# Performance work log

Hardware: AMD Instinct MI355X
Metric: run time of the kernel (lower is better)

The kernel has to match this reference:

```python
import jax, jax.numpy as jnp
import numpy as np

PRIME = 2147483647  # 2^31 - 1, MinHash modulus
GAMMA = 0.3
NUM_HEADS = 8


def minhash_sketch(ids, a, b):
    # ids: (B, L, S) int64 atom ids; a,b: (K,) hash coefficients
    # h[b,l,s,k] = (a[k]*id + b[k]) mod PRIME ; signature = min over the set axis S
    h = (ids[..., None] * a + b) % PRIME          # (B, L, S, K)
    return h.min(axis=2)                          # (B, L, K)


def jaccard_from_signatures(sig_q, sig_k):
    # sig_q: (B, Lq, K), sig_k: (B, Lk, K) -> (B, Lq, Lk) fraction of matching slots.
    # Scan over the K hash slots to avoid materializing a (B,Lq,Lk,K) tensor.
    B, Lq, K = sig_q.shape
    Lk = sig_k.shape[1]

    def step(acc, cols):
        qc, kc = cols                              # (B,Lq), (B,Lk)
        return acc + (qc[:, :, None] == kc[:, None, :]).astype(jnp.float32), None

    init = jnp.zeros((B, Lq, Lk), jnp.float32)
    xs = (jnp.moveaxis(sig_q, -1, 0), jnp.moveaxis(sig_k, -1, 0))
    acc, _ = jax.lax.scan(step, init, xs)
    return acc / K


def symdiff_from_jaccard(jacc, size_q, size_k):
    # |A ∩ B| = J/(1+J) * (|A|+|B|)  =>  |A Δ B| = (|A|+|B|) * (1-J)/(1+J)
    tot = size_q[:, :, None] + size_k[:, None, :]   # (B, Lq, Lk)
    return tot * (1.0 - jacc) / (1.0 + jacc)


def setup_inputs() -> dict:
    key = jax.random.key(0)
    ks = jax.random.split(key, 12)
    B, Lq, Lk, E, S, K, V = 4, 1024, 1024, 512, 8, 128, 32000
    w = lambda k: (jax.random.normal(k, (E, E), jnp.float32) * 0.02)
    return {
        "query": jax.random.normal(ks[0], (B, Lq, E), jnp.float32),
        "key": jax.random.normal(ks[1], (B, Lk, E), jnp.float32),
        "value": jax.random.normal(ks[2], (B, Lk, E), jnp.float32),
        "token_sets_q": jax.random.randint(ks[3], (B, Lq, S), 0, V).astype(jnp.int64),
        "token_sets_k": jax.random.randint(ks[4], (B, Lk, S), 0, V).astype(jnp.int64),
        "hash_a": jax.random.randint(ks[5], (K,), 1, PRIME - 1).astype(jnp.int64),
        "hash_b": jax.random.randint(ks[6], (K,), 0, PRIME - 1).astype(jnp.int64),
        "Wq": w(ks[7]), "bq": jnp.zeros((E,), jnp.float32),
        "Wk": w(ks[8]), "bk": jnp.zeros((E,), jnp.float32),
        "Wv": w(ks[9]), "bv": jnp.zeros((E,), jnp.float32),
        "Wo": w(ks[10]), "bo": jnp.zeros((E,), jnp.float32),
    }


def reference(query, key, value, token_sets_q, token_sets_k, hash_a, hash_b,
              Wq, bq, Wk, bk, Wv, bv, Wo, bo):
    B, Lq, E = query.shape
    Lk = key.shape[1]
    H = NUM_HEADS
    d = E // H

    # in-projections (torch Linear: x @ W^T + b); q,k are computed but the
    # attention scores come solely from the token-set kernel (gating disabled)
    q = query @ Wq.T + bq
    k = key @ Wk.T + bk
    v = (value @ Wv.T + bv).reshape(B, Lk, H, d).transpose(0, 2, 1, 3)  # (B,H,Lk,d)

    # MinHash sketches of per-token atom sets -> estimated Jaccard -> Δ-RBF score
    sig_q = minhash_sketch(token_sets_q, hash_a, hash_b)   # (B,Lq,K)
    sig_k = minhash_sketch(token_sets_k, hash_a, hash_b)   # (B,Lk,K)
    jacc = jaccard_from_signatures(sig_q, sig_k)           # (B,Lq,Lk)

    S = token_sets_q.shape[-1]
    size_q = jnp.full((B, Lq), S, jnp.float32)             # uniform CSR offsets -> |set| = S
    size_k = jnp.full((B, Lk), S, jnp.float32)
    delta = symdiff_from_jaccard(jacc, size_q, size_k)
    scores = jnp.exp(-GAMMA * delta)                       # (B,Lq,Lk), shared by all heads

    attn = jax.nn.softmax(scores, axis=-1)                 # no masks, no causal, dropout=0
    ctx = jnp.einsum('bqk,bhkd->bqhd', attn, v).reshape(B, Lq, E)
    return ctx @ Wo.T + bo
```

## Files before the change

### kernel.cpp

```cpp
#include <hip/hip_runtime.h>
#include <hip/hip_bf16.h>
#include <stdint.h>

#define PRIME 2147483647u
#define GAMMA 0.3f
#define K_HASH 128
#define S_SET 8
#define NB 4
#define LQ 1024
#define LK 1024
#define EDIM 512

typedef unsigned short ushort_t;
typedef __attribute__((ext_vector_type(8))) short short8;
typedef __attribute__((ext_vector_type(4))) float f32x4;

static __device__ __forceinline__ unsigned short f2bf(float f) {
    unsigned u = __builtin_bit_cast(unsigned, f);
    u += 0x7FFFu + ((u >> 16) & 1u);
    return (unsigned short)(u >> 16);
}

static __device__ __forceinline__ void glds16(const void* g, void* l) {
    __builtin_amdgcn_global_load_lds(
        (const __attribute__((address_space(1))) unsigned int*)g,
        (__attribute__((address_space(3))) unsigned int*)l, 16, 0, 0);
}

#define SWZ(r) ((((r) >> 2) & 3) ^ ((r) & 3))

static __device__ __forceinline__ unsigned nm2(unsigned acc, unsigned a,
                                               unsigned b, unsigned ones) {
    unsigned x = a ^ b, t;
    asm("v_pk_min_u16 %0, %1, %2" : "=v"(t) : "v"(x), "v"(ones));
    return acc + t;
}
static __device__ __forceinline__ unsigned nm8(unsigned acc, int4 q, int4 k,
                                               unsigned ones) {
    acc = nm2(acc, (unsigned)q.x, (unsigned)k.x, ones);
    acc = nm2(acc, (unsigned)q.y, (unsigned)k.y, ones);
    acc = nm2(acc, (unsigned)q.z, (unsigned)k.z, ones);
    acc = nm2(acc, (unsigned)q.w, (unsigned)k.w, ones);
    return acc;
}

#define EPI_ROWBIAS  0
#define EPI_ROWDIV   1
#define EPI_COLBIAS  2

template<int OUTF32, int MODE>
static __device__ void gemm64_dev(
        const ushort_t* __restrict__ A, const ushort_t* __restrict__ B,
        void* __restrict__ C,
        const float* __restrict__ bias, const float* __restrict__ scale,
        int lda, int ldb, int ldc, int Kd, int m0, int n0,
        ushort_t* AsBase, ushort_t* BsBase, int tid) {
    ushort_t (*As)[64 * 32] = (ushort_t (*)[64 * 32])AsBase;
    ushort_t (*Bs)[64 * 32] = (ushort_t (*)[64 * 32])BsBase;
    int w = tid >> 6, lane = tid & 63;
    int wm = (w & 1) * 32, wn = (w >> 1) * 32;
    int mrow = lane & 15, kg = lane >> 4;

    int r = tid >> 2, c = (tid & 3) ^ SWZ(r);
    const ushort_t* pa = A + (size_t)(m0 + r) * lda + c * 8;
    const ushort_t* pb = B + (size_t)(n0 + r) * ldb + c * 8;

    int aoff[2], boff[2];
    #pragma unroll
    for (int s = 0; s < 2; s++) {
        int Ra = wm + s * 16 + mrow;
        aoff[s] = Ra * 32 + (kg ^ SWZ(Ra)) * 8;
        int Rb = wn + s * 16 + mrow;
        boff[s] = Rb * 32 + (kg ^ SWZ(Rb)) * 8;
    }

    f32x4 acc[2][2] = {};
    int nK = Kd >> 5;
    glds16(pa, &As[0][tid * 8]);
    glds16(pb, &Bs[0][tid * 8]);
    for (int i = 0; i < nK; i++) {
        __syncthreads();
        int cur = i & 1, nxt = cur ^ 1;
        if (i + 1 < nK) {
            int k0 = (i + 1) << 5;
            glds16(pa + k0, &As[nxt][tid * 8]);
            glds16(pb + k0, &Bs[nxt][tid * 8]);
        }
        short8 af[2], bh[2];
        #pragma unroll
        for (int s = 0; s < 2; s++) {
            af[s] = *(const short8*)&As[cur][aoff[s]];
            bh[s] = *(const short8*)&Bs[cur][boff[s]];
        }
        #pragma unroll
        for (int ii = 0; ii < 2; ii++)
            #pragma unroll
            for (int jj = 0; jj < 2; jj++)
                acc[ii][jj] = __builtin_amdgcn_mfma_f32_16x16x32_bf16(
                                  af[ii], bh[jj], acc[ii][jj], 0, 0, 0);
    }

    int col = lane & 15, rbase = (lane >> 4) * 4;
    #pragma unroll
    for (int ii = 0; ii < 2; ii++) {
        #pragma unroll
        for (int jj = 0; jj < 2; jj++) {
            #pragma unroll
            for (int rr = 0; rr < 4; rr++) {
                int gm = m0 + wm + ii * 16 + rbase + rr;
                int gn = n0 + wn + jj * 16 + col;
                float v = acc[ii][jj][rr];
                if (MODE == EPI_ROWBIAS)     v += bias[gm];
                else if (MODE == EPI_ROWDIV) v /= scale[gm];
                else                         v += bias[gn];
                size_t cix = (size_t)gm * ldc + gn;
                if (OUTF32) ((float*)C)[cix] = v;
                else        ((ushort_t*)C)[cix] = f2bf(v);
            }
        }
    }
}

#define CVT_N0 (NB * LK * EDIM)
#define CVT_N1 (EDIM * EDIM)
#define CVT_N2 (EDIM * EDIM)
#define CVT_BLOCKS ((CVT_N0 + CVT_N1 + CVT_N2) / (256 * 8))
#define SIG_BLOCKS (NB * (LQ + LK) / 2)

__global__ __launch_bounds__(256) void prep_kernel(
        const float* __restrict__ v, const float* __restrict__ wv,
        const float* __restrict__ wo,
        ushort_t* __restrict__ vb, ushort_t* __restrict__ wvb,
        ushort_t* __restrict__ wob,
        const int* __restrict__ ts_q, const int* __restrict__ ts_k,
        const int* __restrict__ ha, const int* __restrict__ hb,
        ushort_t* __restrict__ sig_q, ushort_t* __restrict__ sig_k,
        float* __restrict__ rs) {
    int blk = blockIdx.x;
    if (blk < CVT_BLOCKS) {
        size_t i = ((size_t)blk * 256 + threadIdx.x) * 8;
        const float* src; ushort_t* dst; size_t off;
        if (i < CVT_N0)                { src = v;  dst = vb;  off = i; }
        else if (i < CVT_N0 + CVT_N1)  { src = wv; dst = wvb; off = i - CVT_N0; }
        else                           { src = wo; dst = wob; off = i - CVT_N0 - CVT_N1; }
        float4 a = *(const float4*)(src + off);
        float4 b = *(const float4*)(src + off + 4);
        ushort4 o0, o1;
        o0.x = f2bf(a.x); o0.y = f2bf(a.y); o0.z = f2bf(a.z); o0.w = f2bf(a.w);
        o1.x = f2bf(b.x); o1.y = f2bf(b.y); o1.z = f2bf(b.z); o1.w = f2bf(b.w);
        *(ushort4*)(dst + off)     = o0;
        *(ushort4*)(dst + off + 4) = o1;
        return;
    }
    int sb = blk - CVT_BLOCKS;
    if (sb < 16) rs[sb * 256 + threadIdx.x] = 0.f;
    int half = threadIdx.x >> 7, k = threadIdx.x & 127;
    int row = sb * 2 + half;
    const int* ts = (row < NB * LQ) ? ts_q : ts_k;
    ushort_t* sig = (row < NB * LQ) ? sig_q : sig_k;
    int idx = row & (NB * LQ - 1);
    unsigned long long a  = (unsigned)ha[k];
    unsigned long long bb = (unsigned)hb[k];
    __shared__ int ids[2][S_SET];
    if (k < S_SET) ids[half][k] = ts[idx * S_SET + k];
    __syncthreads();
    unsigned mn = 0xFFFFFFFFu;
    #pragma unroll
    for (int s = 0; s < S_SET; s++) {
        unsigned long long x = a * (unsigned long long)(unsigned)ids[half][s] + bb;
        x = (x & PRIME) + (x >> 31);
        x = (x & PRIME) + (x >> 31);
        unsigned r = (unsigned)x;
        if (r >= PRIME) r -= PRIME;
        mn = (r < mn) ? r : mn;
    }
    sig[idx * K_HASH + k] = (ushort_t)mn;
}

union JacSmem {
    struct {
        int Qs[128 * 36];
        int Ks[64 * 36];
        float lut[K_HASH + 1];
    } jac;
    struct {
        ushort_t As[2][64 * 32];
        ushort_t Bs[2][64 * 32];
    } g;
};

__global__ __launch_bounds__(256) void jacg1_kernel(
        const ushort_t* __restrict__ sig_q, const ushort_t* __restrict__ sig_k,
        ushort_t* __restrict__ P, float* __restrict__ rs,
        const ushort_t* __restrict__ Wvb, const ushort_t* __restrict__ Vb,
        ushort_t* __restrict__ Vt, const float* __restrict__ bv) {
    __shared__ JacSmem sm;
    int blk = blockIdx.x, tid = threadIdx.x;
    int grp = blk >> 8;
    int t = (grp >> 1) * 256 + (blk & 255);
    if (grp & 1) {
        gemm64_dev<0, EPI_ROWBIAS>(Wvb, Vb, Vt, bv, nullptr,
                                   EDIM, EDIM, NB * LK, EDIM,
                                   (t >> 6) * 64, (t & 63) * 64,
                                   sm.g.As[0], sm.g.Bs[0], tid);
        return;
    }
    if (tid <= K_HASH) {
        float r = (float)(K_HASH - tid) / (float)(K_HASH + tid);
        sm.jac.lut[tid] = expf(expf(-GAMMA * (2.0f * S_SET) * r));
    }
    int b = t >> 7;
    int q0 = ((t >> 4) & 7) * 128, j0 = (t & 15) * 64;
    const int4* gq = (const int4*)(sig_q + ((size_t)b * LQ + q0) * K_HASH);
    const int4* gk = (const int4*)(sig_k + ((size_t)b * LK + j0) * K_HASH);
    int tx = tid & 15, ty = tid >> 4;
    unsigned ones = 0x00010001u;
    unsigned acc[8][4] = {};
    int sra = tid >> 2, srb = 64 + sra, sg0 = (tid & 3) * 2;
    #pragma unroll 1
    for (int h = 0; h < 2; h++) {
        __syncthreads();
        #pragma unroll
        for (int u = 0; u < 2; u++) {
            int g = sg0 + u;
            *(int4*)&sm.jac.Qs[sra * 36 + ((g ^ (sra >> 2)) & 7) * 4]
                = gq[sra * 16 + h * 8 + g];
            *(int4*)&sm.jac.Qs[srb * 36 + ((g ^ (srb >> 2)) & 7) * 4]
                = gq[srb * 16 + h * 8 + g];
            *(int4*)&sm.jac.Ks[sra * 36 + ((g ^ (sra >> 2)) & 7) * 4]
                = gk[sra * 16 + h * 8 + g];
        }
        __syncthreads();
        #pragma unroll
        for (int g = 0; g < 8; g++) {
            int4 qv[8], kv[4];
            #pragma unroll
            for (int i = 0; i < 8; i++) {
                int r = ty * 8 + i;
                qv[i] = *(const int4*)&sm.jac.Qs[r * 36 + ((g ^ (r >> 2)) & 7) * 4];
            }
            #pragma unroll
            for (int j = 0; j < 4; j++) {
                int r = tx * 4 + j;
                kv[j] = *(const int4*)&sm.jac.Ks[r * 36 + ((g ^ (r >> 2)) & 7) * 4];
            }
            #pragma unroll
            for (int i = 0; i < 8; i++)
                #pragma unroll
                for (int j = 0; j < 4; j++)
                    acc[i][j] = nm8(acc[i][j], qv[i], kv[j], ones);
        }
    }
    ushort_t* Pb = P + (size_t)b * LQ * LK;
    float fsum[8];
    #pragma unroll
    for (int i = 0; i < 8; i++) {
        ushort4 o;
        unsigned n0_ = (acc[i][0] & 0xFFFFu) + (acc[i][0] >> 16);
        unsigned n1_ = (acc[i][1] & 0xFFFFu) + (acc[i][1] >> 16);
        unsigned n2_ = (acc[i][2] & 0xFFFFu) + (acc[i][2] >> 16);
        unsigned n3_ = (acc[i][3] & 0xFFFFu) + (acc[i][3] >> 16);
        float p0 = sm.jac.lut[K_HASH - n0_], p1 = sm.jac.lut[K_HASH - n1_];
        float p2 = sm.jac.lut[K_HASH - n2_], p3 = sm.jac.lut[K_HASH - n3_];
        fsum[i] = (p0 + p1) + (p2 + p3);
        o.x = f2bf(p0); o.y = f2bf(p1); o.z = f2bf(p2); o.w = f2bf(p3);
        int row = q0 + ty * 8 + i;
        *(ushort4*)&Pb[(size_t)row * LK + j0 + tx * 4] = o;
    }
    __syncthreads();
    float* fs = (float*)&sm.jac.Qs[0];
    #pragma unroll
    for (int i = 0; i < 8; i++) fs[(ty * 8 + i) * 16 + tx] = fsum[i];
    __syncthreads();
    if (tid < 128) {
        float s = 0.f;
        #pragma unroll
        for (int tt = 0; tt < 16; tt++) s += fs[tid * 16 + tt];
        atomicAdd(&rs[(size_t)b * LQ + q0 + tid], s);
    }
}

template<int OUTF32, int MODE>
__global__ __launch_bounds__(256) void btgemm_kernel(
        const ushort_t* __restrict__ A, const ushort_t* __restrict__ B,
        void* __restrict__ C,
        const float* __restrict__ bias, const float* __restrict__ scale,
        int lda, int ldb, int ldc, int Kd,
        long long sA, long long sB, long long sC, long long sS) {
    __shared__ ushort_t As[2][64 * 32], Bs[2][64 * 32];
    int z = blockIdx.z;
    gemm64_dev<OUTF32, MODE>(
        A + (size_t)z * sA, B + (size_t)z * sB,
        (char*)C + (size_t)z * sC * (OUTF32 ? 4 : 2),
        bias, scale + (size_t)z * sS,
        lda, ldb, ldc, Kd, blockIdx.y * 64, blockIdx.x * 64,
        As[0], Bs[0], threadIdx.x);
}

extern "C" void kernel_launch(void* const* d_in, const int* in_sizes, int n_in,
                              void* d_out, int out_size, void* d_ws, size_t ws_size,
                              hipStream_t stream) {
    const float* value = (const float*)d_in[2];
    const int* tsq = (const int*)d_in[3];
    const int* tsk = (const int*)d_in[4];
    const int* ha  = (const int*)d_in[5];
    const int* hb  = (const int*)d_in[6];
    const float* Wv = (const float*)d_in[11];
    const float* bv = (const float*)d_in[12];
    const float* Wo = (const float*)d_in[13];
    const float* bo = (const float*)d_in[14];
    float* out = (float*)d_out;

    char* ws = (char*)d_ws;
    ushort_t* sigq   = (ushort_t*)(ws);
    ushort_t* sigk   = (ushort_t*)(ws + (1ull << 20));
    ushort_t* P      = (ushort_t*)(ws + (4ull << 20));
    float* rs        = (float*)(ws + (12ull << 20));
    ushort_t* Vt     = (ushort_t*)(ws + (12ull << 20) + (1ull << 16));
    ushort_t* ctx    = (ushort_t*)(ws + (17ull << 20));
    ushort_t* Vb     = (ushort_t*)(ws + (21ull << 20));
    ushort_t* Wvb    = (ushort_t*)(ws + (25ull << 20));
    ushort_t* Wob    = (ushort_t*)(ws + (25ull << 20) + (512ull << 10));

    prep_kernel<<<CVT_BLOCKS + SIG_BLOCKS, 256, 0, stream>>>(
        value, Wv, Wo, Vb, Wvb, Wob, tsq, tsk, ha, hb, sigq, sigk, rs);

    jacg1_kernel<<<1024, 256, 0, stream>>>(sigq, sigk, P, rs, Wvb, Vb, Vt, bv);

    btgemm_kernel<0, EPI_ROWDIV><<<dim3(EDIM / 64, LQ / 64, NB), 256, 0, stream>>>(
        P, Vt, ctx, bv , rs,
        LK, NB * LK, EDIM, LK,
        (long long)LQ * LK, (long long)LK, (long long)LQ * EDIM, (long long)LQ);

    btgemm_kernel<1, EPI_COLBIAS><<<dim3(EDIM / 64, NB * LQ / 64, 1), 256, 0, stream>>>(
        ctx, Wob, out, bo, rs ,
        EDIM, EDIM, EDIM, EDIM, 0LL, 0LL, 0LL, 0LL);
}
```

Measured before the change: 153.8 us.

## Replace all-pairs MinHash comparison with per-slot hash join match counting

Signatures are now stored as full 32-bit values. Instead of comparing every query/key pair across all 128 slots, each block builds a shared-memory hash table of the key signatures for one (batch, slot) and probes it with the query values, atomically incrementing byte counters in a zeroed match matrix. A separate kernel turns the counts into bf16 probabilities through a lookup table and computes row sums without global atomics. This removes the dense O(Lq·Lk·K) comparison work, since random signatures rarely match. The cost is an extra kernel, a 4 MB zero-fill and count read-back, and atomic contention whenever the data has many collisions.

Result: no change. 151.4 us (-1.6%).

```diff
diff --git a/kernel.cpp b/kernel.cpp
--- a/kernel.cpp
+++ b/kernel.cpp
@@ -28,21 +28,6 @@
 }
 
 #define SWZ(r) ((((r) >> 2) & 3) ^ ((r) & 3))
-
-static __device__ __forceinline__ unsigned nm2(unsigned acc, unsigned a,
-                                               unsigned b, unsigned ones) {
-    unsigned x = a ^ b, t;
-    asm("v_pk_min_u16 %0, %1, %2" : "=v"(t) : "v"(x), "v"(ones));
-    return acc + t;
-}
-static __device__ __forceinline__ unsigned nm8(unsigned acc, int4 q, int4 k,
-                                               unsigned ones) {
-    acc = nm2(acc, (unsigned)q.x, (unsigned)k.x, ones);
-    acc = nm2(acc, (unsigned)q.y, (unsigned)k.y, ones);
-    acc = nm2(acc, (unsigned)q.z, (unsigned)k.z, ones);
-    acc = nm2(acc, (unsigned)q.w, (unsigned)k.w, ones);
-    return acc;
-}
 
 #define EPI_ROWBIAS  0
 #define EPI_ROWDIV   1
@@ -125,6 +110,7 @@
 #define CVT_N1 (EDIM * EDIM)
 #define CVT_N2 (EDIM * EDIM)
 #define CVT_BLOCKS ((CVT_N0 + CVT_N1 + CVT_N2) / (256 * 8))
+#define MZ_BLOCKS 1024
 #define SIG_BLOCKS (NB * (LQ + LK) / 2)
 
 __global__ __launch_bounds__(256) void prep_kernel(
@@ -134,8 +120,8 @@
         ushort_t* __restrict__ wob,
         const int* __restrict__ ts_q, const int* __restrict__ ts_k,
         const int* __restrict__ ha, const int* __restrict__ hb,
-        ushort_t* __restrict__ sig_q, ushort_t* __restrict__ sig_k,
-        float* __restrict__ rs) {
+        unsigned* __restrict__ sig_q, unsigned* __restrict__ sig_k,
+        uint8_t* __restrict__ Mz) {
     int blk = blockIdx.x;
     if (blk < CVT_BLOCKS) {
         size_t i = ((size_t)blk * 256 + threadIdx.x) * 8;
@@ -152,12 +138,16 @@
         *(ushort4*)(dst + off + 4) = o1;
         return;
     }
-    int sb = blk - CVT_BLOCKS;
-    if (sb < 16) rs[sb * 256 + threadIdx.x] = 0.f;
+    if (blk < CVT_BLOCKS + MZ_BLOCKS) {
+        size_t off = ((size_t)(blk - CVT_BLOCKS) * 256 + threadIdx.x) * 16;
+        *(int4*)(Mz + off) = (int4){0, 0, 0, 0};
+        return;
+    }
+    int sb = blk - CVT_BLOCKS - MZ_BLOCKS;
     int half = threadIdx.x >> 7, k = threadIdx.x & 127;
     int row = sb * 2 + half;
     const int* ts = (row < NB * LQ) ? ts_q : ts_k;
-    ushort_t* sig = (row < NB * LQ) ? sig_q : sig_k;
+    unsigned* sig = (row < NB * LQ) ? sig_q : sig_k;
     int idx = row & (NB * LQ - 1);
     unsigned long long a  = (unsigned)ha[k];
     unsigned long long bb = (unsigned)hb[k];
@@ -174,110 +164,83 @@
         if (r >= PRIME) r -= PRIME;
         mn = (r < mn) ? r : mn;
     }
-    sig[idx * K_HASH + k] = (ushort_t)mn;
-}
-
-union JacSmem {
-    struct {
-        int Qs[128 * 36];
-        int Ks[64 * 36];
-        float lut[K_HASH + 1];
-    } jac;
-    struct {
-        ushort_t As[2][64 * 32];
-        ushort_t Bs[2][64 * 32];
-    } g;
+    sig[idx * K_HASH + k] = mn;
+}
+
+union JSmem {
+    struct { unsigned keys[2048]; ushort_t vals[2048]; } j;
+    struct { ushort_t As[2][64 * 32]; ushort_t Bs[2][64 * 32]; } g;
 };
 
-__global__ __launch_bounds__(256) void jacg1_kernel(
-        const ushort_t* __restrict__ sig_q, const ushort_t* __restrict__ sig_k,
-        ushort_t* __restrict__ P, float* __restrict__ rs,
+__global__ __launch_bounds__(256) void joing1_kernel(
+        const unsigned* __restrict__ sig_q, const unsigned* __restrict__ sig_k,
+        uint8_t* __restrict__ M,
         const ushort_t* __restrict__ Wvb, const ushort_t* __restrict__ Vb,
         ushort_t* __restrict__ Vt, const float* __restrict__ bv) {
-    __shared__ JacSmem sm;
+    __shared__ JSmem sm;
     int blk = blockIdx.x, tid = threadIdx.x;
-    int grp = blk >> 8;
-    int t = (grp >> 1) * 256 + (blk & 255);
-    if (grp & 1) {
+    int t = blk & 511;
+    if ((blk >> 9) == 0) {
         gemm64_dev<0, EPI_ROWBIAS>(Wvb, Vb, Vt, bv, nullptr,
                                    EDIM, EDIM, NB * LK, EDIM,
                                    (t >> 6) * 64, (t & 63) * 64,
                                    sm.g.As[0], sm.g.Bs[0], tid);
         return;
     }
+    int b = t >> 7, k = t & 127;
+    for (int i = tid; i < 2048; i += 256) sm.j.keys[i] = 0xFFFFFFFFu;
+    __syncthreads();
+    const unsigned* skc = sig_k + (size_t)b * LK * K_HASH + k;
+    const unsigned* sqc = sig_q + (size_t)b * LQ * K_HASH + k;
+    for (int u = 0; u < 4; u++) {
+        int j = u * 256 + tid;
+        unsigned vv = skc[(size_t)j * K_HASH];
+        unsigned h = (vv * 2654435761u) >> 21;
+        while (true) {
+            unsigned prev = atomicCAS(&sm.j.keys[h], 0xFFFFFFFFu, vv);
+            if (prev == 0xFFFFFFFFu) { sm.j.vals[h] = (ushort_t)j; break; }
+            h = (h + 1) & 2047;
+        }
+    }
+    __syncthreads();
+    uint8_t* Mb = M + ((size_t)b << 20);
+    for (int u = 0; u < 4; u++) {
+        int q = u * 256 + tid;
+        unsigned vv = sqc[(size_t)q * K_HASH];
+        unsigned h = (vv * 2654435761u) >> 21;
+        unsigned kk;
+        while ((kk = sm.j.keys[h]) != 0xFFFFFFFFu) {
+            if (kk == vv) {
+                unsigned ix = ((unsigned)q << 10) + sm.j.vals[h];
+                atomicAdd((unsigned*)(Mb + (ix & ~3u)), 1u << ((ix & 3u) * 8));
+            }
+            h = (h + 1) & 2047;
+        }
+    }
+}
+
+__global__ __launch_bounds__(256) void lutrs_kernel(
+        const uint8_t* __restrict__ M, ushort_t* __restrict__ P,
+        float* __restrict__ rs) {
+    __shared__ float lut[K_HASH + 1];
+    __shared__ float wsum[4];
+    int row = blockIdx.x, tid = threadIdx.x;
     if (tid <= K_HASH) {
         float r = (float)(K_HASH - tid) / (float)(K_HASH + tid);
-        sm.jac.lut[tid] = expf(expf(-GAMMA * (2.0f * S_SET) * r));
-    }
-    int b = t >> 7;
-    int q0 = ((t >> 4) & 7) * 128, j0 = (t & 15) * 64;
-    const int4* gq = (const int4*)(sig_q + ((size_t)b * LQ + q0) * K_HASH);
-    const int4* gk = (const int4*)(sig_k + ((size_t)b * LK + j0) * K_HASH);
-    int tx = tid & 15, ty = tid >> 4;
-    unsigned ones = 0x00010001u;
-    unsigned acc[8][4] = {};
-    int sra = tid >> 2, srb = 64 + sra, sg0 = (tid & 3) * 2;
-    #pragma unroll 1
-    for (int h = 0; h < 2; h++) {
-        __syncthreads();
-        #pragma unroll
-        for (int u = 0; u < 2; u++) {
-            int g = sg0 + u;
-            *(int4*)&sm.jac.Qs[sra * 36 + ((g ^ (sra >> 2)) & 7) * 4]
-                = gq[sra * 16 + h * 8 + g];
-            *(int4*)&sm.jac.Qs[srb * 36 + ((g ^ (srb >> 2)) & 7) * 4]
-                = gq[srb * 16 + h * 8 + g];
-            *(int4*)&sm.jac.Ks[sra * 36 + ((g ^ (sra >> 2)) & 7) * 4]
-                = gk[sra * 16 + h * 8 + g];
-        }
-        __syncthreads();
-        #pragma unroll
-        for (int g = 0; g < 8; g++) {
-            int4 qv[8], kv[4];
-            #pragma unroll
-            for (int i = 0; i < 8; i++) {
-                int r = ty * 8 + i;
-                qv[i] = *(const int4*)&sm.jac.Qs[r * 36 + ((g ^ (r >> 2)) & 7) * 4];
-            }
-            #pragma unroll
-            for (int j = 0; j < 4; j++) {
-                int r = tx * 4 + j;
-                kv[j] = *(const int4*)&sm.jac.Ks[r * 36 + ((g ^ (r >> 2)) & 7) * 4];
-            }
-            #pragma unroll
-            for (int i = 0; i < 8; i++)
-                #pragma unroll
-                for (int j = 0; j < 4; j++)
-                    acc[i][j] = nm8(acc[i][j], qv[i], kv[j], ones);
-        }
-    }
-    ushort_t* Pb = P + (size_t)b * LQ * LK;
-    float fsum[8];
+        lut[tid] = expf(expf(-GAMMA * (2.0f * S_SET) * r));
+    }
+    __syncthreads();
+    uchar4 m4 = *(const uchar4*)(M + (size_t)row * LK + tid * 4);
+    float p0 = lut[m4.x], p1 = lut[m4.y], p2 = lut[m4.z], p3 = lut[m4.w];
+    ushort4 o;
+    o.x = f2bf(p0); o.y = f2bf(p1); o.z = f2bf(p2); o.w = f2bf(p3);
+    *(ushort4*)(P + (size_t)row * LK + tid * 4) = o;
+    float s = (p0 + p1) + (p2 + p3);
     #pragma unroll
-    for (int i = 0; i < 8; i++) {
-        ushort4 o;
-        unsigned n0_ = (acc[i][0] & 0xFFFFu) + (acc[i][0] >> 16);
-        unsigned n1_ = (acc[i][1] & 0xFFFFu) + (acc[i][1] >> 16);
-        unsigned n2_ = (acc[i][2] & 0xFFFFu) + (acc[i][2] >> 16);
-        unsigned n3_ = (acc[i][3] & 0xFFFFu) + (acc[i][3] >> 16);
-        float p0 = sm.jac.lut[K_HASH - n0_], p1 = sm.jac.lut[K_HASH - n1_];
-        float p2 = sm.jac.lut[K_HASH - n2_], p3 = sm.jac.lut[K_HASH - n3_];
-        fsum[i] = (p0 + p1) + (p2 + p3);
-        o.x = f2bf(p0); o.y = f2bf(p1); o.z = f2bf(p2); o.w = f2bf(p3);
-        int row = q0 + ty * 8 + i;
-        *(ushort4*)&Pb[(size_t)row * LK + j0 + tx * 4] = o;
-    }
-    __syncthreads();
-    float* fs = (float*)&sm.jac.Qs[0];
-    #pragma unroll
-    for (int i = 0; i < 8; i++) fs[(ty * 8 + i) * 16 + tx] = fsum[i];
-    __syncthreads();
-    if (tid < 128) {
-        float s = 0.f;
-        #pragma unroll
-        for (int tt = 0; tt < 16; tt++) s += fs[tid * 16 + tt];
-        atomicAdd(&rs[(size_t)b * LQ + q0 + tid], s);
-    }
+    for (int off = 32; off; off >>= 1) s += __shfl_down(s, off);
+    if ((tid & 63) == 0) wsum[tid >> 6] = s;
+    __syncthreads();
+    if (tid == 0) rs[row] = (wsum[0] + wsum[1]) + (wsum[2] + wsum[3]);
 }
 
 template<int OUTF32, int MODE>
@@ -312,20 +275,23 @@
     float* out = (float*)d_out;
 
     char* ws = (char*)d_ws;
-    ushort_t* sigq   = (ushort_t*)(ws);
-    ushort_t* sigk   = (ushort_t*)(ws + (1ull << 20));
-    ushort_t* P      = (ushort_t*)(ws + (4ull << 20));
-    float* rs        = (float*)(ws + (12ull << 20));
-    ushort_t* Vt     = (ushort_t*)(ws + (12ull << 20) + (1ull << 16));
-    ushort_t* ctx    = (ushort_t*)(ws + (17ull << 20));
-    ushort_t* Vb     = (ushort_t*)(ws + (21ull << 20));
-    ushort_t* Wvb    = (ushort_t*)(ws + (25ull << 20));
-    ushort_t* Wob    = (ushort_t*)(ws + (25ull << 20) + (512ull << 10));
-
-    prep_kernel<<<CVT_BLOCKS + SIG_BLOCKS, 256, 0, stream>>>(
-        value, Wv, Wo, Vb, Wvb, Wob, tsq, tsk, ha, hb, sigq, sigk, rs);
-
-    jacg1_kernel<<<1024, 256, 0, stream>>>(sigq, sigk, P, rs, Wvb, Vb, Vt, bv);
+    unsigned* sigq = (unsigned*)(ws);
+    unsigned* sigk = (unsigned*)(ws + (2ull << 20));
+    uint8_t*  M    = (uint8_t*)(ws + (4ull << 20));
+    ushort_t* P    = (ushort_t*)(ws + (8ull << 20));
+    float*    rs   = (float*)(ws + (16ull << 20));
+    ushort_t* Vt   = (ushort_t*)(ws + (16ull << 20) + (64ull << 10));
+    ushort_t* ctx  = (ushort_t*)(ws);
+    ushort_t* Vb   = (ushort_t*)(ws + (20ull << 20) + (64ull << 10));
+    ushort_t* Wvb  = (ushort_t*)(ws + (24ull << 20) + (64ull << 10));
+    ushort_t* Wob  = (ushort_t*)(ws + (24ull << 20) + (64ull << 10) + (512ull << 10));
+
+    prep_kernel<<<CVT_BLOCKS + MZ_BLOCKS + SIG_BLOCKS, 256, 0, stream>>>(
+        value, Wv, Wo, Vb, Wvb, Wob, tsq, tsk, ha, hb, sigq, sigk, M);
+
+    joing1_kernel<<<1024, 256, 0, stream>>>(sigq, sigk, M, Wvb, Vb, Vt, bv);
+
+    lutrs_kernel<<<NB * LQ, 256, 0, stream>>>(M, P, rs);
 
     btgemm_kernel<0, EPI_ROWDIV><<<dim3(EDIM / 64, LQ / 64, NB), 256, 0, stream>>>(
         P, Vt, ctx, bv , rs,
```
